# Optimization experiments

Hardware: AMD Instinct MI355X
Metric: run time of the kernel (lower is better)

## Reference

```python
import jax, jax.numpy as jnp
import numpy as np

B, FMAX, H, LF, LC = 512, 16, 128, 64, 256
TAU, BIAS = 1000000.0, 1.0


def _gru(x, W_ih, W_hh, b_ih, b_hh):
    # x: [N, L, H]; torch GRU gate order (r, z, n)
    def step(h, xt):
        gi = xt @ W_ih.T + b_ih            # [N, 3H]
        gh = h @ W_hh.T + b_hh
        ir, iz, in_ = jnp.split(gi, 3, axis=-1)
        hr, hz, hn = jnp.split(gh, 3, axis=-1)
        r = jax.nn.sigmoid(ir + hr)
        z = jax.nn.sigmoid(iz + hz)
        n = jnp.tanh(in_ + r * hn)
        h_new = (1.0 - z) * n + z * h
        return h_new, h_new
    h0 = jnp.zeros((x.shape[0], W_hh.shape[1]), x.dtype)
    _, hs = jax.lax.scan(step, h0, jnp.swapaxes(x, 0, 1))
    return jnp.swapaxes(hs, 0, 1)          # [N, L, H]


def setup_inputs() -> dict:
    key = jax.random.key(0)
    ks = jax.random.split(key, 12)
    counts = (np.arange(B) % FMAX) + 1      # group sizes, max == FMAX
    N = int(counts.sum())                   # 4352
    user_idx = np.repeat(np.arange(B), counts).astype(np.int32)
    offsets = np.concatenate([[0], np.cumsum(counts)])
    gather_idx = np.zeros((B, FMAX), np.int32)
    pad_mask = np.zeros((B, FMAX), np.int32)
    for b in range(B):
        c = counts[b]
        gather_idx[b, :c] = offsets[b] + np.arange(c)
        pad_mask[b, :c] = 1
    lf = (np.arange(N) % LF) + 1
    friend_src_mask = (np.arange(LF)[None, :] < lf[:, None]).astype(np.int32)
    lc = (np.arange(N) % LC) + 1
    common_src_mask = (np.arange(LC)[None, :] < lc[:, None]).astype(np.int32)
    s = 1.0 / np.sqrt(H)
    return {
        "self_x": jax.random.normal(ks[0], (B, H), jnp.float32),
        "common_x": jax.random.normal(ks[1], (N, LC, H), jnp.float32),
        "common_time": jax.random.uniform(ks[2], (N, LC), jnp.float32) * 1e6,
        "friend_x": jax.random.normal(ks[3], (N, LF, H), jnp.float32),
        "W_ih": jax.random.uniform(ks[4], (3 * H, H), jnp.float32, -s, s),
        "W_hh": jax.random.uniform(ks[5], (3 * H, H), jnp.float32, -s, s),
        "b_ih": jax.random.uniform(ks[6], (3 * H,), jnp.float32, -s, s),
        "b_hh": jax.random.uniform(ks[7], (3 * H,), jnp.float32, -s, s),
        "W_friend": jax.random.uniform(ks[8], (H, 2 * H), jnp.float32, -s, s),
        "W_beta": jax.random.uniform(ks[9], (H, H), jnp.float32, -s, s),
        "friend_src_mask": jnp.asarray(friend_src_mask),
        "common_src_mask": jnp.asarray(common_src_mask),
        "user_idx": jnp.asarray(user_idx),
        "gather_idx": jnp.asarray(gather_idx),
        "pad_mask": jnp.asarray(pad_mask),
    }


def reference(self_x, common_x, common_time, friend_x, W_ih, W_hh, b_ih, b_hh,
              W_friend, W_beta, friend_src_mask, common_src_mask, user_idx,
              gather_idx, pad_mask):
    # --- FRIENDRNN: GRU encode, take last valid step per friend ---
    hs = _gru(friend_x, W_ih, W_hh, b_ih, b_hh)                 # [N, LF, H]
    fmask = friend_src_mask.astype(hs.dtype)
    hs = hs * fmask[..., None]
    idx_last = (friend_src_mask.sum(axis=1) - 1).astype(jnp.int32)  # [N]
    friend_out = jnp.take_along_axis(hs, idx_last[:, None, None], axis=1)[:, 0, :]  # [N, H]

    # --- FRIENDSHIP: temporal-decayed content attention over common items ---
    self_rep = self_x[user_idx]                                  # [N, H]
    sf = jnp.concatenate([self_rep, friend_out], axis=-1) @ W_friend.T  # [N, H]
    proj_common = common_x @ W_beta.T                            # [N, LC, H]
    scores = jnp.einsum('nlh,nh->nl', proj_common, sf)           # [N, LC]
    content = jax.nn.softplus(scores)
    temporal = jnp.exp(-common_time / TAU + BIAS)
    tf = jnp.sum(content * temporal * common_src_mask.astype(content.dtype), axis=-1)  # [N]

    # --- pad to groups (zeros, matching pad_sequence), softmax-weighted agg ---
    pm = pad_mask.astype(tf.dtype)                               # [B, FMAX]
    tf_pad = tf[gather_idx] * pm                                 # [B, FMAX]
    fx_pad = friend_out[gather_idx] * pm[..., None]              # [B, FMAX, H]
    w = jax.nn.softmax(tf_pad, axis=-1)                          # over padded zeros too (faithful)
    return jnp.sum(w[..., None] * fx_pad, axis=1)                # [B, H]
```

## Files before the change

### kernel.cpp

```cpp
#include <hip/hip_runtime.h>
#include <hip/hip_bf16.h>

typedef float float4v __attribute__((ext_vector_type(4)));
typedef __bf16 bf16x8 __attribute__((ext_vector_type(8)));

#define MFMA16(a, b, c) __builtin_amdgcn_mfma_f32_16x16x32_bf16(a, b, c, 0, 0, 0)

__device__ __forceinline__ float fsigmoid(float x) {
    return __builtin_amdgcn_rcpf(1.0f + __expf(-x));
}
__device__ __forceinline__ float ftanh_(float x) {
    float e = __expf(2.0f * x);
    return 1.0f - 2.0f * __builtin_amdgcn_rcpf(e + 1.0f);
}
__device__ __forceinline__ float softplusf(float x) {
    return fmaxf(x, 0.0f) + __logf(1.0f + __expf(-fabsf(x)));
}

#define STAGE(U0, U1, XHd, XLd) {                                              \
    bf16x8 fh, fl;                                                             \
    _Pragma("unroll")                                                          \
    for (int j = 0; j < 4; ++j) {                                              \
        __bf16 h0 = (__bf16)(U0)[j]; fh[j] = h0;                               \
        fl[j] = (__bf16)((U0)[j] - (float)h0);                                 \
        __bf16 h1 = (__bf16)(U1)[j]; fh[j + 4] = h1;                           \
        fl[j + 4] = (__bf16)((U1)[j] - (float)h1);                             \
    }                                                                          \
    *(bf16x8*)&(XHd)[tid * 8] = fh;                                            \
    *(bf16x8*)&(XLd)[tid * 8] = fl;                                            \
}

#define X_PHASE(XHp, XLp)                                                      \
    _Pragma("unroll")                                                          \
    for (int c = 0; c < 4; ++c) {                                              \
        const int fo_ = (c * 64 + lane) * 8;                                   \
        bf16x8 xh = *(const bf16x8*)&(XHp)[fo_];                               \
        bf16x8 xl = *(const bf16x8*)&(XLp)[fo_];                               \
        _Pragma("unroll")                                                      \
        for (int ct = 0; ct < 2; ++ct) {                                       \
            nR[ct]  = MFMA16(xh, wihh[0][ct][c], nR[ct]);                      \
            nR[ct]  = MFMA16(xl, wihh[0][ct][c], nR[ct]);                      \
            nR[ct]  = MFMA16(xh, wihl[0][ct][c], nR[ct]);                      \
            nZ[ct]  = MFMA16(xh, wihh[1][ct][c], nZ[ct]);                      \
            nZ[ct]  = MFMA16(xl, wihh[1][ct][c], nZ[ct]);                      \
            nZ[ct]  = MFMA16(xh, wihl[1][ct][c], nZ[ct]);                      \
            nIN[ct] = MFMA16(xh, wihh[2][ct][c], nIN[ct]);                     \
            nIN[ct] = MFMA16(xl, wihh[2][ct][c], nIN[ct]);                     \
            nIN[ct] = MFMA16(xh, wihl[2][ct][c], nIN[ct]);                     \
        }                                                                      \
    }

#define NEXT_INIT()                                                            \
    _Pragma("unroll")                                                          \
    for (int ct = 0; ct < 2; ++ct) {                                           \
        nR[ct]  = (float4v){biasR[ct],  biasR[ct],  biasR[ct],  biasR[ct]};    \
        nZ[ct]  = (float4v){biasZ[ct],  biasZ[ct],  biasZ[ct],  biasZ[ct]};    \
        nIN[ct] = (float4v){biasIN[ct], biasIN[ct], biasIN[ct], biasIN[ct]};   \
    }

__global__ __launch_bounds__(256, 1)
void gru_kernel(const float* __restrict__ friend_x,
                const float* __restrict__ W_ih, const float* __restrict__ W_hh,
                const float* __restrict__ b_ih, const float* __restrict__ b_hh,
                const int* __restrict__ fmask,
                float* __restrict__ friend_out)
{
    __shared__ __align__(16) __bf16 lds[8 * 2048];
    __shared__ int s_lf[16];
    __shared__ int s_n[16];

    const int tid = threadIdx.x;
    const int wv = tid >> 6;
    const int lane = tid & 63;
    const int cn = lane & 15;
    const int qq = lane >> 4;

    __bf16* const XH0 = lds;
    __bf16* const XH1 = lds + 2048;
    __bf16* const XL0 = lds + 2 * 2048;
    __bf16* const XL1 = lds + 3 * 2048;
    __bf16* const HH0 = lds + 4 * 2048;
    __bf16* const HH1 = lds + 5 * 2048;
    __bf16* const HL0 = lds + 6 * 2048;
    __bf16* const HL1 = lds + 7 * 2048;

    if (tid < 16) {
        const int p = blockIdx.x * 16 + tid;
        const int v = p / 68;
        const int j = p - v * 68;
        const int n = (63 - v) + 64 * j;
        s_n[tid] = n;
        const int* mp = fmask + (long)n * 64;
        int s = 0;
        for (int i = 0; i < 64; ++i) s += mp[i];
        s_lf[tid] = s;
    }

    {
        bf16x8 z8;
#pragma unroll
        for (int j = 0; j < 8; ++j) z8[j] = (__bf16)0.0f;
        for (int i = tid; i < 4 * 2048 / 8; i += 256) ((bf16x8*)HH0)[i] = z8;
    }

    bf16x8 wihh[3][2][4], wihl[3][2][4], whhh[3][2][4], whhl[3][2][4];
#pragma unroll
    for (int gate = 0; gate < 3; ++gate)
#pragma unroll
        for (int ct = 0; ct < 2; ++ct) {
            const int row = gate * 128 + wv * 32 + ct * 16 + cn;
#pragma unroll
            for (int c = 0; c < 4; ++c) {
                const float* p = W_ih + row * 128 + c * 32 + qq * 8;
                float4v u0 = *(const float4v*)p;
                float4v u1 = *(const float4v*)(p + 4);
                bf16x8 fh, fl;
#pragma unroll
                for (int j = 0; j < 4; ++j) {
                    __bf16 h0 = (__bf16)u0[j]; fh[j] = h0; fl[j] = (__bf16)(u0[j] - (float)h0);
                    __bf16 h1 = (__bf16)u1[j]; fh[j + 4] = h1; fl[j + 4] = (__bf16)(u1[j] - (float)h1);
                }
                wihh[gate][ct][c] = fh; wihl[gate][ct][c] = fl;
                const float* q = W_hh + row * 128 + c * 32 + qq * 8;
                float4v v0 = *(const float4v*)q;
                float4v v1 = *(const float4v*)(q + 4);
                bf16x8 gh, gl;
#pragma unroll
                for (int j = 0; j < 4; ++j) {
                    __bf16 h0 = (__bf16)v0[j]; gh[j] = h0; gl[j] = (__bf16)(v0[j] - (float)h0);
                    __bf16 h1 = (__bf16)v1[j]; gh[j + 4] = h1; gl[j + 4] = (__bf16)(v1[j] - (float)h1);
                }
                whhh[gate][ct][c] = gh; whhl[gate][ct][c] = gl;
            }
        }

    float biasR[2], biasZ[2], biasIN[2], biasHN[2];
#pragma unroll
    for (int ct = 0; ct < 2; ++ct) {
        const int cc = wv * 32 + ct * 16 + cn;
        biasR[ct] = b_ih[cc] + b_hh[cc];
        biasZ[ct] = b_ih[128 + cc] + b_hh[128 + cc];
        biasIN[ct] = b_ih[256 + cc];
        biasHN[ct] = b_hh[256 + cc];
    }

    __syncthreads();

    const int srow = lane & 15;
    const int ss = lane >> 4;
    const float* xp = friend_x + (long)s_n[srow] * 8192 + wv * 32 + ss * 8;

    int lfA[4], nA[4];
#pragma unroll
    for (int r = 0; r < 4; ++r) { lfA[r] = s_lf[qq * 4 + r]; nA[r] = s_n[qq * 4 + r]; }
    int maxlf = 0;
    for (int i = 0; i < 16; ++i) maxlf = (s_lf[i] > maxlf) ? s_lf[i] : maxlf;

    {
        float4v a0 = *(const float4v*)(xp);
        float4v a1 = *(const float4v*)(xp + 4);
        float4v b0 = *(const float4v*)(xp + 128);
        float4v b1 = *(const float4v*)(xp + 132);
        STAGE(a0, a1, XH0, XL0);
        STAGE(b0, b1, XH1, XL1);
    }
    __syncthreads();

    float4v nR[2], nZ[2], nIN[2];
    NEXT_INIT();
    X_PHASE(XH0, XL0);
    __syncthreads();

    float hC[2][4];
#pragma unroll
    for (int ct = 0; ct < 2; ++ct)
#pragma unroll
        for (int r = 0; r < 4; ++r) hC[ct][r] = 0.0f;

    for (int t = 0; t < maxlf; ++t) {
        const int cur = t & 1;
        __bf16* const HHc = cur ? HH1 : HH0;
        __bf16* const HLc = cur ? HL1 : HL0;
        __bf16* const XHr = cur ? XH0 : XH1;
        __bf16* const XLr = cur ? XL0 : XL1;
        __bf16* const XHw = cur ? XH1 : XH0;
        __bf16* const XLw = cur ? XL1 : XL0;
        __bf16* const HHn = cur ? HH0 : HH1;
        __bf16* const HLn = cur ? HL0 : HL1;

        const bool pf2 = (t + 2 < maxlf);
        float4v u0, u1;
        if (pf2) {
            u0 = *(const float4v*)(xp + (t + 2) * 128);
            u1 = *(const float4v*)(xp + (t + 2) * 128 + 4);
        }

        float4v aR[2], aZ[2], aIN[2], aHN[2];
#pragma unroll
        for (int ct = 0; ct < 2; ++ct) {
            aR[ct] = nR[ct]; aZ[ct] = nZ[ct]; aIN[ct] = nIN[ct];
            aHN[ct] = (float4v){biasHN[ct], biasHN[ct], biasHN[ct], biasHN[ct]};
        }

#pragma unroll
        for (int c = 0; c < 4; ++c) {
            const int fo_ = (c * 64 + lane) * 8;
            bf16x8 hh = *(const bf16x8*)&HHc[fo_];
            bf16x8 hl = *(const bf16x8*)&HLc[fo_];
#pragma unroll
            for (int ct = 0; ct < 2; ++ct) {
                aR[ct]  = MFMA16(hh, whhh[0][ct][c], aR[ct]);
                aR[ct]  = MFMA16(hl, whhh[0][ct][c], aR[ct]);
                aR[ct]  = MFMA16(hh, whhl[0][ct][c], aR[ct]);
                aZ[ct]  = MFMA16(hh, whhh[1][ct][c], aZ[ct]);
                aZ[ct]  = MFMA16(hl, whhh[1][ct][c], aZ[ct]);
                aZ[ct]  = MFMA16(hh, whhl[1][ct][c], aZ[ct]);
                aHN[ct] = MFMA16(hh, whhh[2][ct][c], aHN[ct]);
                aHN[ct] = MFMA16(hl, whhh[2][ct][c], aHN[ct]);
                aHN[ct] = MFMA16(hh, whhl[2][ct][c], aHN[ct]);
            }
        }

        const bool hasNext = (t + 1 < maxlf);
        if (hasNext) {
            NEXT_INIT();
            X_PHASE(XHr, XLr);
        }

        if (pf2) {
            STAGE(u0, u1, XHw, XLw);
        }

#pragma unroll
        for (int ct = 0; ct < 2; ++ct) {
            const int col = wv * 32 + ct * 16 + cn;
            const int c2 = col >> 5, s2 = (col >> 3) & 3, j2 = col & 7;
#pragma unroll
            for (int reg = 0; reg < 4; ++reg) {
                const int row = qq * 4 + reg;
                float r = fsigmoid(aR[ct][reg]);
                float z = fsigmoid(aZ[ct][reg]);
                float nn = ftanh_(aIN[ct][reg] + r * aHN[ct][reg]);
                float h = (1.0f - z) * nn + z * hC[ct][reg];
                hC[ct][reg] = h;
                __bf16 hhi = (__bf16)h;
                __bf16 hlo = (__bf16)(h - (float)hhi);
                const int sl = (c2 * 64 + row + 16 * s2) * 8 + j2;
                HHn[sl] = hhi;
                HLn[sl] = hlo;
                if (t + 1 == lfA[reg])
                    friend_out[(long)nA[reg] * 128 + col] = h;
            }
        }

        __syncthreads();
    }
}

__global__ __launch_bounds__(256)
void attn_kernel(const float* __restrict__ self_x,
                 const float* __restrict__ common_x,
                 const float* __restrict__ common_time,
                 const float* __restrict__ W_friend,
                 const float* __restrict__ W_beta,
                 const int* __restrict__ csm,
                 const int* __restrict__ user_idx,
                 const float* __restrict__ friend_out,
                 float* __restrict__ tf)
{
    const int n = blockIdx.x;
    const int tid = threadIdx.x;
    const int wv = tid >> 6, lane = tid & 63;
    __shared__ __align__(16) float catf[256];
    __shared__ float sfs[128];
    __shared__ __align__(16) float vv[128];
    __shared__ float vpart[2][128];
    __shared__ int lcp[4];
    __shared__ int s_lc;
    __shared__ float wsum[4];

    if (tid < 128) catf[tid] = self_x[user_idx[n] * 128 + tid];
    else           catf[tid] = friend_out[(long)n * 128 + tid - 128];

    int mv = csm[(long)n * 256 + tid];
#pragma unroll
    for (int o = 32; o; o >>= 1) mv += __shfl_down(mv, o);
    if (lane == 0) lcp[wv] = mv;
    __syncthreads();
    if (tid == 0) s_lc = lcp[0] + lcp[1] + lcp[2] + lcp[3];

    float4v c4 = *(const float4v*)&catf[4 * lane];
    for (int i = 0; i < 32; ++i) {
        const int h = wv * 32 + i;
        float4v w4 = *(const float4v*)(W_friend + h * 256 + 4 * lane);
        float p = w4[0] * c4[0] + w4[1] * c4[1] + w4[2] * c4[2] + w4[3] * c4[3];
#pragma unroll
        for (int o = 1; o < 64; o <<= 1) p += __shfl_xor(p, o);
        if (lane == 0) sfs[h] = p;
    }
    __syncthreads();

    {
        const int col = tid & 127, half = tid >> 7;
        float acc = 0.f;
#pragma unroll 4
        for (int kk = 0; kk < 64; ++kk) {
            const int hh = kk * 2 + half;
            acc += sfs[hh] * W_beta[hh * 128 + col];
        }
        vpart[half][col] = acc;
    }
    __syncthreads();
    if (tid < 128) vv[tid] = vpart[0][tid] + vpart[1][tid];
    __syncthreads();

    const int lc = s_lc;
    const int lh = lane & 31, sub = lane >> 5;
    float4v v4 = *(const float4v*)&vv[4 * lh];
    const float* cxn = common_x + (long)n * 32768 + 4 * lh;
    const float* ctn = common_time + (long)n * 256;
    float acc = 0.f;
#pragma unroll 4
    for (int l0 = wv * 2 + sub; l0 < lc; l0 += 8) {
        float4v x4 = *(const float4v*)(cxn + l0 * 128);
        float p = x4[0] * v4[0] + x4[1] * v4[1] + x4[2] * v4[2] + x4[3] * v4[3];
#pragma unroll
        for (int o = 1; o < 32; o <<= 1) p += __shfl_xor(p, o);
        float contrib = softplusf(p) * __expf(1.0f - ctn[l0] * 1e-6f);
        if (lh == 0) acc += contrib;
    }
    acc += __shfl_xor(acc, 32);
    if (lane == 0) wsum[wv] = acc;
    __syncthreads();
    if (tid == 0) tf[n] = wsum[0] + wsum[1] + wsum[2] + wsum[3];
}

__global__ __launch_bounds__(128)
void agg_kernel(const float* __restrict__ tf, const float* __restrict__ fo,
                const int* __restrict__ gather_idx, const int* __restrict__ pad_mask,
                float* __restrict__ out)
{
    const int b = blockIdx.x, tid = threadIdx.x;
    __shared__ float tfp[16];
    __shared__ int gidx[16];
    __shared__ float pmf[16];
    if (tid < 16) {
        const int gg = gather_idx[b * 16 + tid];
        const int pp = pad_mask[b * 16 + tid];
        gidx[tid] = gg; pmf[tid] = (float)pp;
        tfp[tid] = pp ? tf[gg] : 0.0f;
    }
    __syncthreads();
    float m = tfp[0];
#pragma unroll
    for (int f = 1; f < 16; ++f) m = fmaxf(m, tfp[f]);
    float e[16]; float s = 0.f;
#pragma unroll
    for (int f = 0; f < 16; ++f) { e[f] = __expf(tfp[f] - m); s += e[f]; }
    const float inv = 1.0f / s;
    float acc = 0.f;
#pragma unroll
    for (int f = 0; f < 16; ++f) {
        if (pmf[f] != 0.0f) {
            const float w = e[f] * inv;
            acc += w * fo[(long)gidx[f] * 128 + tid];
        }
    }
    out[b * 128 + tid] = acc;
}

extern "C" void kernel_launch(void* const* d_in, const int* in_sizes, int n_in,
                              void* d_out, int out_size, void* d_ws, size_t ws_size,
                              hipStream_t stream)
{
    const float* self_x      = (const float*)d_in[0];
    const float* common_x    = (const float*)d_in[1];
    const float* common_time = (const float*)d_in[2];
    const float* friend_x    = (const float*)d_in[3];
    const float* W_ih        = (const float*)d_in[4];
    const float* W_hh        = (const float*)d_in[5];
    const float* b_ih        = (const float*)d_in[6];
    const float* b_hh        = (const float*)d_in[7];
    const float* W_friend    = (const float*)d_in[8];
    const float* W_beta      = (const float*)d_in[9];
    const int* fmask         = (const int*)d_in[10];
    const int* csm           = (const int*)d_in[11];
    const int* uidx          = (const int*)d_in[12];
    const int* gidx          = (const int*)d_in[13];
    const int* pmask         = (const int*)d_in[14];
    float* out = (float*)d_out;

    const int N = in_sizes[12];
    const int B = in_sizes[0] / 128;

    float* fo_ws = (float*)d_ws;
    float* tf_ws = fo_ws + (size_t)N * 128;

    gru_kernel<<<(N + 15) / 16, 256, 0, stream>>>(friend_x, W_ih, W_hh, b_ih, b_hh,
                                                  fmask, fo_ws);
    attn_kernel<<<N, 256, 0, stream>>>(self_x, common_x, common_time,
                                       W_friend, W_beta, csm, uidx, fo_ws, tf_ws);
    agg_kernel<<<B, 128, 0, stream>>>(tf_ws, fo_ws, gidx, pmask, out);

    (void)n_in; (void)out_size; (void)ws_size;
}
```

Before: 1.028 ms.

## Batch per-row friend/beta projections into a separate MFMA kernel

Moves the sf = [self,friend]·W_friendᵀ and v = sf·W_beta matvecs out of the per-row attention kernel into a new proj_kernel. It handles 16 rows per block using bf16 MFMA, with a three-way bf16 split so the results stay close to fp32. The attention kernel then just loads the precomputed v vector per row. This avoids every block re-reading both weight matrices and running serial shuffle reductions. The cost is an extra launch, a workspace round trip for v, and the extra MFMA work from the split-precision scheme.

After: 995.6 us. 3.2% less time.

```diff
diff --git a/kernel.cpp b/kernel.cpp
--- a/kernel.cpp
+++ b/kernel.cpp
@@ -257,66 +257,185 @@
     }
 }
 
-__global__ __launch_bounds__(256)
-void attn_kernel(const float* __restrict__ self_x,
-                 const float* __restrict__ common_x,
-                 const float* __restrict__ common_time,
+__device__ __forceinline__ void tsplit8(const float4v u0, const float4v u1,
+                                        bf16x8& fh, bf16x8& fm, bf16x8& fl)
+{
+#pragma unroll
+    for (int j = 0; j < 4; ++j) {
+        float x0 = u0[j];
+        __bf16 h0 = (__bf16)x0; float r0 = x0 - (float)h0;
+        __bf16 m0 = (__bf16)r0; float s0 = r0 - (float)m0;
+        fh[j] = h0; fm[j] = m0; fl[j] = (__bf16)s0;
+        float x1 = u1[j];
+        __bf16 h1 = (__bf16)x1; float r1 = x1 - (float)h1;
+        __bf16 m1 = (__bf16)r1; float s1 = r1 - (float)m1;
+        fh[j + 4] = h1; fm[j + 4] = m1; fl[j + 4] = (__bf16)s1;
+    }
+}
+
+__global__ __launch_bounds__(256, 1)
+void proj_kernel(const float* __restrict__ self_x,
+                 const float* __restrict__ friend_out,
                  const float* __restrict__ W_friend,
                  const float* __restrict__ W_beta,
+                 const int* __restrict__ user_idx,
+                 float* __restrict__ vws)
+{
+    __shared__ __align__(16) __bf16 catH[4096], catM[4096], catL[4096];
+    __shared__ __align__(16) __bf16 sfH[2048], sfM[2048], sfL[2048];
+
+    const int tid = threadIdx.x;
+    const int wv = tid >> 6;
+    const int lane = tid & 63;
+    const int cn = lane & 15;
+    const int qq = lane >> 4;
+    const int n0 = blockIdx.x * 16;
+
+    {
+        const int srow = lane & 15;
+        const int ss = lane >> 4;
+        const int n_r = n0 + srow;
+        const int k = wv * 32 + ss * 8;
+        const float* ps = self_x + (long)user_idx[n_r] * 128 + k;
+        float4v a0 = *(const float4v*)ps;
+        float4v a1 = *(const float4v*)(ps + 4);
+        bf16x8 fh, fm, fl;
+        tsplit8(a0, a1, fh, fm, fl);
+        *(bf16x8*)&catH[tid * 8] = fh;
+        *(bf16x8*)&catM[tid * 8] = fm;
+        *(bf16x8*)&catL[tid * 8] = fl;
+        const float* pf = friend_out + (long)n_r * 128 + k;
+        float4v b0 = *(const float4v*)pf;
+        float4v b1 = *(const float4v*)(pf + 4);
+        tsplit8(b0, b1, fh, fm, fl);
+        *(bf16x8*)&catH[(tid + 256) * 8] = fh;
+        *(bf16x8*)&catM[(tid + 256) * 8] = fm;
+        *(bf16x8*)&catL[(tid + 256) * 8] = fl;
+    }
+
+    bf16x8 wfh[2][8], wfm[2][8], wfl[2][8];
+#pragma unroll
+    for (int ct = 0; ct < 2; ++ct) {
+        const int hcol = wv * 32 + ct * 16 + cn;
+#pragma unroll
+        for (int c = 0; c < 8; ++c) {
+            const float* p = W_friend + hcol * 256 + c * 32 + qq * 8;
+            float4v u0 = *(const float4v*)p;
+            float4v u1 = *(const float4v*)(p + 4);
+            tsplit8(u0, u1, wfh[ct][c], wfm[ct][c], wfl[ct][c]);
+        }
+    }
+
+    bf16x8 wbh[2][4], wbm[2][4], wbl[2][4];
+#pragma unroll
+    for (int ct = 0; ct < 2; ++ct) {
+        const int colN = wv * 32 + ct * 16 + cn;
+#pragma unroll
+        for (int c = 0; c < 4; ++c) {
+            float4v u0, u1;
+#pragma unroll
+            for (int j = 0; j < 4; ++j) {
+                u0[j] = W_beta[(c * 32 + qq * 8 + j) * 128 + colN];
+                u1[j] = W_beta[(c * 32 + qq * 8 + 4 + j) * 128 + colN];
+            }
+            tsplit8(u0, u1, wbh[ct][c], wbm[ct][c], wbl[ct][c]);
+        }
+    }
+
+    __syncthreads();
+
+    float4v sA[2];
+#pragma unroll
+    for (int ct = 0; ct < 2; ++ct) sA[ct] = (float4v){0.f, 0.f, 0.f, 0.f};
+#pragma unroll
+    for (int c = 0; c < 8; ++c) {
+        const int fo_ = (c * 64 + lane) * 8;
+        bf16x8 ah = *(const bf16x8*)&catH[fo_];
+        bf16x8 am = *(const bf16x8*)&catM[fo_];
+        bf16x8 al = *(const bf16x8*)&catL[fo_];
+#pragma unroll
+        for (int ct = 0; ct < 2; ++ct) {
+            sA[ct] = MFMA16(ah, wfh[ct][c], sA[ct]);
+            sA[ct] = MFMA16(ah, wfm[ct][c], sA[ct]);
+            sA[ct] = MFMA16(am, wfh[ct][c], sA[ct]);
+            sA[ct] = MFMA16(am, wfm[ct][c], sA[ct]);
+            sA[ct] = MFMA16(ah, wfl[ct][c], sA[ct]);
+            sA[ct] = MFMA16(al, wfh[ct][c], sA[ct]);
+        }
+    }
+
+#pragma unroll
+    for (int ct = 0; ct < 2; ++ct) {
+        const int col = wv * 32 + ct * 16 + cn;
+        const int c2 = col >> 5, s2 = (col >> 3) & 3, j2 = col & 7;
+#pragma unroll
+        for (int reg = 0; reg < 4; ++reg) {
+            const int row = qq * 4 + reg;
+            const int sl = (c2 * 64 + row + 16 * s2) * 8 + j2;
+            float x = sA[ct][reg];
+            __bf16 h = (__bf16)x; float r1 = x - (float)h;
+            __bf16 m = (__bf16)r1; float r2 = r1 - (float)m;
+            sfH[sl] = h; sfM[sl] = m; sfL[sl] = (__bf16)r2;
+        }
+    }
+    __syncthreads();
+
+    float4v vA[2];
+#pragma unroll
+    for (int ct = 0; ct < 2; ++ct) vA[ct] = (float4v){0.f, 0.f, 0.f, 0.f};
+#pragma unroll
+    for (int c = 0; c < 4; ++c) {
+        const int fo_ = (c * 64 + lane) * 8;
+        bf16x8 ah = *(const bf16x8*)&sfH[fo_];
+        bf16x8 am = *(const bf16x8*)&sfM[fo_];
+        bf16x8 al = *(const bf16x8*)&sfL[fo_];
+#pragma unroll
+        for (int ct = 0; ct < 2; ++ct) {
+            vA[ct] = MFMA16(ah, wbh[ct][c], vA[ct]);
+            vA[ct] = MFMA16(ah, wbm[ct][c], vA[ct]);
+            vA[ct] = MFMA16(am, wbh[ct][c], vA[ct]);
+            vA[ct] = MFMA16(am, wbm[ct][c], vA[ct]);
+            vA[ct] = MFMA16(ah, wbl[ct][c], vA[ct]);
+            vA[ct] = MFMA16(al, wbh[ct][c], vA[ct]);
+        }
+    }
+
+#pragma unroll
+    for (int ct = 0; ct < 2; ++ct) {
+        const int col = wv * 32 + ct * 16 + cn;
+#pragma unroll
+        for (int reg = 0; reg < 4; ++reg) {
+            const int row = qq * 4 + reg;
+            vws[(long)(n0 + row) * 128 + col] = vA[ct][reg];
+        }
+    }
+}
+
+__global__ __launch_bounds__(256)
+void attn_kernel(const float* __restrict__ common_x,
+                 const float* __restrict__ common_time,
                  const int* __restrict__ csm,
-                 const int* __restrict__ user_idx,
-                 const float* __restrict__ friend_out,
+                 const float* __restrict__ vws,
                  float* __restrict__ tf)
 {
     const int n = blockIdx.x;
     const int tid = threadIdx.x;
     const int wv = tid >> 6, lane = tid & 63;
-    __shared__ __align__(16) float catf[256];
-    __shared__ float sfs[128];
-    __shared__ __align__(16) float vv[128];
-    __shared__ float vpart[2][128];
     __shared__ int lcp[4];
     __shared__ int s_lc;
     __shared__ float wsum[4];
 
-    if (tid < 128) catf[tid] = self_x[user_idx[n] * 128 + tid];
-    else           catf[tid] = friend_out[(long)n * 128 + tid - 128];
-
     int mv = csm[(long)n * 256 + tid];
 #pragma unroll
     for (int o = 32; o; o >>= 1) mv += __shfl_down(mv, o);
     if (lane == 0) lcp[wv] = mv;
     __syncthreads();
     if (tid == 0) s_lc = lcp[0] + lcp[1] + lcp[2] + lcp[3];
-
-    float4v c4 = *(const float4v*)&catf[4 * lane];
-    for (int i = 0; i < 32; ++i) {
-        const int h = wv * 32 + i;
-        float4v w4 = *(const float4v*)(W_friend + h * 256 + 4 * lane);
-        float p = w4[0] * c4[0] + w4[1] * c4[1] + w4[2] * c4[2] + w4[3] * c4[3];
-#pragma unroll
-        for (int o = 1; o < 64; o <<= 1) p += __shfl_xor(p, o);
-        if (lane == 0) sfs[h] = p;
-    }
-    __syncthreads();
-
-    {
-        const int col = tid & 127, half = tid >> 7;
-        float acc = 0.f;
-#pragma unroll 4
-        for (int kk = 0; kk < 64; ++kk) {
-            const int hh = kk * 2 + half;
-            acc += sfs[hh] * W_beta[hh * 128 + col];
-        }
-        vpart[half][col] = acc;
-    }
-    __syncthreads();
-    if (tid < 128) vv[tid] = vpart[0][tid] + vpart[1][tid];
     __syncthreads();
 
     const int lc = s_lc;
     const int lh = lane & 31, sub = lane >> 5;
-    float4v v4 = *(const float4v*)&vv[4 * lh];
+    float4v v4 = *(const float4v*)(vws + (long)n * 128 + 4 * lh);
     const float* cxn = common_x + (long)n * 32768 + 4 * lh;
     const float* ctn = common_time + (long)n * 256;
     float acc = 0.f;
@@ -395,11 +514,13 @@
 
     float* fo_ws = (float*)d_ws;
     float* tf_ws = fo_ws + (size_t)N * 128;
+    float* v_ws  = tf_ws + (size_t)N;
 
     gru_kernel<<<(N + 15) / 16, 256, 0, stream>>>(friend_x, W_ih, W_hh, b_ih, b_hh,
                                                   fmask, fo_ws);
-    attn_kernel<<<N, 256, 0, stream>>>(self_x, common_x, common_time,
-                                       W_friend, W_beta, csm, uidx, fo_ws, tf_ws);
+    proj_kernel<<<N / 16, 256, 0, stream>>>(self_x, fo_ws, W_friend, W_beta,
+                                            uidx, v_ws);
+    attn_kernel<<<N, 256, 0, stream>>>(common_x, common_time, csm, v_ws, tf_ws);
     agg_kernel<<<B, 128, 0, stream>>>(tf_ws, fo_ws, gidx, pmask, out);
 
     (void)n_in; (void)out_size; (void)ws_size;
```
